# Kernel optimization log

Hardware: AMD Instinct MI355X
Metric: run time of the kernel (lower is better)

## Reference

```python
import jax, jax.numpy as jnp
import numpy as np

N_NODES = 100000
N_EDGES = 1600000
NUM_GRAPHS = 4096
HID = 128
F_IN = 11
F_OUT = 19


def setup_inputs() -> dict:
    key = jax.random.key(0)
    ks = jax.random.split(key, 8)
    x = jax.random.normal(ks[0], (N_NODES, F_IN), dtype=jnp.float32)
    edge_src = jax.random.randint(ks[1], (N_EDGES,), 0, N_NODES)
    edge_dst = jax.random.randint(ks[2], (N_EDGES,), 0, N_NODES)
    batch = jnp.sort(jax.random.randint(ks[3], (N_NODES,), 0, NUM_GRAPHS))
    W1 = jax.random.normal(ks[4], (F_IN, HID), dtype=jnp.float32) / np.sqrt(F_IN)
    b1 = jnp.zeros((HID,), dtype=jnp.float32)
    W2 = jax.random.normal(ks[5], (HID, HID), dtype=jnp.float32) / np.sqrt(HID)
    b2 = jnp.zeros((HID,), dtype=jnp.float32)
    Wlin = jax.random.normal(ks[6], (HID, F_OUT), dtype=jnp.float32) / np.sqrt(HID)
    blin = jnp.zeros((F_OUT,), dtype=jnp.float32)
    return {"x": x, "edge_src": edge_src, "edge_dst": edge_dst, "batch": batch,
            "W1": W1, "b1": b1, "W2": W2, "b2": b2, "Wlin": Wlin, "blin": blin}


def _gcn_conv(x, W, b, src, dst, norm, n_nodes):
    # x: [N, Fin] -> h: [N, Fout]; gather-normalize-scatter over edges (self-loops included in src/dst/norm)
    h = x @ W
    msgs = h[src] * norm[:, None]              # [E+N, Fout]
    out = jax.ops.segment_sum(msgs, dst, num_segments=n_nodes)
    return out + b


def reference(x, edge_src, edge_dst, batch, W1, b1, W2, b2, Wlin, blin):
    n = x.shape[0]
    # add self-loops (GCNConv default)
    loops = jnp.arange(n)
    src = jnp.concatenate([edge_src, loops])
    dst = jnp.concatenate([edge_dst, loops])
    # symmetric normalization deg^-1/2[src] * deg^-1/2[dst], deg computed on dst with self-loops
    deg = jax.ops.segment_sum(jnp.ones_like(dst, dtype=x.dtype), dst, num_segments=n)
    dinv = jnp.where(deg > 0, jax.lax.rsqrt(deg), 0.0)
    norm = dinv[src] * dinv[dst]
    h = _gcn_conv(x, W1, b1, src, dst, norm, n)
    h = jax.nn.relu(h)
    h = _gcn_conv(h, W2, b2, src, dst, norm, n)
    # global mean pool over batch assignment
    sums = jax.ops.segment_sum(h, batch, num_segments=NUM_GRAPHS)
    cnts = jax.ops.segment_sum(jnp.ones((n,), dtype=h.dtype), batch, num_segments=NUM_GRAPHS)
    pooled = sums / jnp.maximum(cnts, 1.0)[:, None]   # [NUM_GRAPHS, HID]
    return pooled @ Wlin + blin                       # [NUM_GRAPHS, F_OUT]
```

## Files before the change

kernel.cpp:

```cpp
#include <hip/hip_runtime.h>
#include <hip/hip_fp16.h>

#define N_NODES 100000
#define N_EDGES 1600000
#define NUM_G   4096
#define HID     128
#define F_IN    11
#define F_PAD   16
#define F_OUT   19

#define NB      256
#define KPB     391
#define BCAP    8192
#define GCAP    1024
#define P01_EPB 2048
#define NREG    8
#define REGW    12500
#define GPB     4
#define NAGG    782
#define CH_G    8

__device__ inline void acc_row_f16(float* acc, uint4 u, float w) {
    const __half2* hp = (const __half2*)&u;
#pragma unroll
    for (int i = 0; i < 4; ++i) {
        acc[2 * i]     += __half2float(__low2half(hp[i]))  * w;
        acc[2 * i + 1] += __half2float(__high2half(hp[i])) * w;
    }
}
__device__ inline void add_row_f16(float* acc, uint4 u) {
    const __half2* hp = (const __half2*)&u;
#pragma unroll
    for (int i = 0; i < 4; ++i) {
        acc[2 * i]     += __half2float(__low2half(hp[i]));
        acc[2 * i + 1] += __half2float(__high2half(hp[i]));
    }
}

__global__ void p1_place(const int* __restrict__ src, const int* __restrict__ dst,
                         int* __restrict__ bcur, unsigned int* __restrict__ ebuf) {
    __shared__ int h[NB];
    __shared__ int base[NB];
    h[threadIdx.x] = 0;
    __syncthreads();
    unsigned int pk[8]; int bn[8];
    int b0 = blockIdx.x * P01_EPB;
    int e8 = b0 + threadIdx.x * 8;
    if (e8 + 8 <= N_EDGES) {
        int4 s0 = *(const int4*)(src + e8);
        int4 s1 = *(const int4*)(src + e8 + 4);
        int4 d0 = *(const int4*)(dst + e8);
        int4 d1 = *(const int4*)(dst + e8 + 4);
        int ss[8] = { s0.x, s0.y, s0.z, s0.w, s1.x, s1.y, s1.z, s1.w };
        int dd[8] = { d0.x, d0.y, d0.z, d0.w, d1.x, d1.y, d1.z, d1.w };
#pragma unroll
        for (int k = 0; k < 8; ++k) {
            bn[k] = dd[k] / KPB;
            pk[k] = ((unsigned)ss[k] << 9) | (unsigned)(dd[k] - bn[k] * KPB);
        }
    } else {
#pragma unroll
        for (int k = 0; k < 8; ++k) {
            int e = e8 + k;
            if (e < N_EDGES) {
                int d = dst[e];
                bn[k] = d / KPB;
                pk[k] = ((unsigned)src[e] << 9) | (unsigned)(d - bn[k] * KPB);
            } else bn[k] = -1;
        }
    }
#pragma unroll
    for (int k = 0; k < 8; ++k)
        if (bn[k] >= 0) atomicAdd(&h[bn[k]], 1);
    __syncthreads();
    {
        int c = h[threadIdx.x];
        base[threadIdx.x] = c ? atomicAdd(&bcur[threadIdx.x], c) : 0;
    }
    __syncthreads();
    h[threadIdx.x] = 0;
    __syncthreads();
#pragma unroll
    for (int k = 0; k < 8; ++k) {
        if (bn[k] >= 0) {
            int r = atomicAdd(&h[bn[k]], 1);
            ebuf[(size_t)bn[k] * BCAP + base[bn[k]] + r] = pk[k];
        }
    }
}

__global__ void p2_build(const unsigned int* __restrict__ ebuf, const int* __restrict__ bcur,
                         const float* __restrict__ x,
                         int* __restrict__ row_ptr, int* __restrict__ deg,
                         int* __restrict__ col, float* __restrict__ wd,
                         float* __restrict__ dinv, __half* __restrict__ xp) {
    __shared__ int hist[512];
    __shared__ float ldinv[512];
    __shared__ int wsum[8];
    __shared__ int woff[8];
    int b  = blockIdx.x;
    int t  = threadIdx.x;
    int dbase = b * KPB;
    int nd = N_NODES - dbase; if (nd > KPB) nd = KPB;
    hist[t] = 0;
    __syncthreads();
    int e0 = b * BCAP;
    int e1 = e0 + bcur[b];
    for (int e = e0 + t; e < e1; e += 512)
        atomicAdd(&hist[ebuf[e] & 511u], 1);
    __syncthreads();
    int v = hist[t];
    int lane = t & 63, wv = t >> 6;
    int sv = v;
#pragma unroll
    for (int off = 1; off < 64; off <<= 1) {
        int n = __shfl_up(sv, off, 64);
        if (lane >= off) sv += n;
    }
    if (lane == 63) wsum[wv] = sv;
    __syncthreads();
    if (t == 0) {
        int run = 0;
#pragma unroll
        for (int w = 0; w < 8; ++w) { woff[w] = run; run += wsum[w]; }
    }
    __syncthreads();
    int excl = sv - v + woff[wv];
    float di = rsqrtf(1.0f + (float)v);
    ldinv[t] = di;
    if (t < nd) {
        row_ptr[dbase + t] = e0 + excl;
        deg[dbase + t]     = v;
        dinv[dbase + t]    = di;
    }
    __syncthreads();
    hist[t] = e0 + excl;
    __syncthreads();
    for (int e = e0 + t; e < e1; e += 512) {
        unsigned int w = ebuf[e];
        int dl = (int)(w & 511u);
        int pos = atomicAdd(&hist[dl], 1);
        col[pos] = (int)(w >> 9);
        wd[pos]  = ldinv[dl];
    }
    for (int idx = t; idx < nd * F_PAD; idx += 512) {
        int vl = idx >> 4, f = idx & 15;
        int gv = dbase + vl;
        xp[(size_t)gv * F_PAD + f] =
            __float2half_rn((f < F_IN) ? ldinv[vl] * x[(size_t)gv * F_IN + f] : 0.f);
    }
}

__global__ void agg_es8(const __half* __restrict__ xp, const int* __restrict__ row_ptr,
                        const int* __restrict__ deg, const int* __restrict__ col,
                        const float* __restrict__ dinv,
                        const float* __restrict__ W1, const float* __restrict__ b1,
                        __half* __restrict__ Bh,
                        const int* __restrict__ batch, const float* __restrict__ wd,
                        uint2* __restrict__ ewp, int* __restrict__ gro,
                        int* __restrict__ gb) {
    __shared__ __align__(16) float xs[128][F_PAD];
    __shared__ float W1s[F_IN * HID];
    __shared__ float b1s[HID];
    __shared__ float ds[128];
    __shared__ int cnt[NREG];
    __shared__ int cur[NREG];
    __shared__ int range[2];
    int tid = threadIdx.x;

    if (blockIdx.x < NAGG) {
        for (int i = tid; i < F_IN * HID; i += 256) W1s[i] = W1[i];
        if (tid < HID) b1s[tid] = b1[tid];
        const uint4* xp4 = (const uint4*)xp;
        int v0   = blockIdx.x * 128;
        int v    = v0 + (tid >> 1);
        int lane = tid & 1;
        if (v < N_NODES) {
            if (lane == 0) ds[tid >> 1] = dinv[v];
            float a[8];
#pragma unroll
            for (int k = 0; k < 8; ++k) a[k] = 0.f;
            add_row_f16(a, xp4[(size_t)v * 2 + lane]);
            int j = row_ptr[v], end = j + deg[v];
            int nfull = (end - j) >> 3;
            if (nfull > 0) {
                int cc[8];
#pragma unroll
                for (int k = 0; k < 8; ++k) cc[k] = col[j + k];
                for (int c = 1; c < nfull; ++c) {
                    int nn[8];
#pragma unroll
                    for (int k = 0; k < 8; ++k) nn[k] = col[j + 8 * c + k];
                    uint4 u[8];
#pragma unroll
                    for (int k = 0; k < 8; ++k) u[k] = xp4[(size_t)cc[k] * 2 + lane];
#pragma unroll
                    for (int k = 0; k < 8; ++k) add_row_f16(a, u[k]);
#pragma unroll
                    for (int k = 0; k < 8; ++k) cc[k] = nn[k];
                }
                uint4 u[8];
#pragma unroll
                for (int k = 0; k < 8; ++k) u[k] = xp4[(size_t)cc[k] * 2 + lane];
#pragma unroll
                for (int k = 0; k < 8; ++k) add_row_f16(a, u[k]);
                j += nfull * 8;
            }
            for (; j + 3 < end; j += 4) {
                int s0 = col[j], s1 = col[j + 1], s2 = col[j + 2], s3 = col[j + 3];
                uint4 u0 = xp4[(size_t)s0 * 2 + lane];
                uint4 u1 = xp4[(size_t)s1 * 2 + lane];
                uint4 u2 = xp4[(size_t)s2 * 2 + lane];
                uint4 u3 = xp4[(size_t)s3 * 2 + lane];
                add_row_f16(a, u0); add_row_f16(a, u1);
                add_row_f16(a, u2); add_row_f16(a, u3);
            }
            for (; j < end; ++j)
                add_row_f16(a, xp4[(size_t)col[j] * 2 + lane]);
#pragma unroll
            for (int k = 0; k < 8; ++k) xs[tid >> 1][lane * 8 + k] = a[k];
        }
        __syncthreads();
        int jf   = tid & 127;
        int half = tid >> 7;
        float w[F_IN];
#pragma unroll
        for (int k = 0; k < F_IN; ++k) w[k] = W1s[k * HID + jf];
        float bb = b1s[jf];
        int nmax = N_NODES - v0; if (nmax > 128) nmax = 128;
        for (int n = half; n < nmax; n += 2) {
            const float4* xr = (const float4*)xs[n];
            float4 x0 = xr[0], x1 = xr[1], x2 = xr[2];
            float a = x0.x * w[0] + x0.y * w[1] + x0.z * w[2] + x0.w * w[3]
                    + x1.x * w[4] + x1.y * w[5] + x1.z * w[6] + x1.w * w[7]
                    + x2.x * w[8] + x2.y * w[9] + x2.z * w[10];
            float dv = ds[n];
            float h = fmaxf(dv * a + bb, 0.f);
            Bh[(size_t)(v0 + n) * HID + jf] = __float2half_rn(dv * h);
        }
    } else {
        int g = blockIdx.x - NAGG;
        if (tid < NREG) cnt[tid] = 0;
        if (tid < 2) {
            int tgt = g + tid;
            int lo = 0, hi = N_NODES;
            while (lo < hi) { int m = (lo + hi) >> 1; if (batch[m] < tgt) lo = m + 1; else hi = m; }
            range[tid] = lo;
        }
        __syncthreads();
        int r0 = range[0], r1 = range[1];
        if (tid == 0) {
            gb[g] = r0;
            if (g == NUM_G - 1) gb[NUM_G] = N_NODES;
        }
        int bb0 = 0, bb1 = -1;
        if (r1 > r0) { bb0 = r0 / KPB; bb1 = (r1 - 1) / KPB; }
        for (int bb = bb0; bb <= bb1; ++bb) {
            int vlo = r0 > bb * KPB ? r0 : bb * KPB;
            int vhi = r1 < bb * KPB + KPB ? r1 : bb * KPB + KPB;
            int ee0 = row_ptr[vlo];
            int ee1 = row_ptr[vhi - 1] + deg[vhi - 1];
            for (int e = ee0 + tid; e < ee1; e += 256)
                atomicAdd(&cnt[(unsigned)col[e] / REGW], 1);
        }
        for (int v = r0 + tid; v < r1; v += 256)
            atomicAdd(&cnt[(unsigned)v / REGW], 1);
        __syncthreads();
        if (tid == 0) {
            int run = g * GCAP;
#pragma unroll
            for (int p = 0; p < NREG; ++p) {
                gro[g * 9 + p] = run;
                cur[p] = run;
                run += cnt[p];
            }
            gro[g * 9 + 8] = run;
        }
        __syncthreads();
        for (int bb = bb0; bb <= bb1; ++bb) {
            int vlo = r0 > bb * KPB ? r0 : bb * KPB;
            int vhi = r1 < bb * KPB + KPB ? r1 : bb * KPB + KPB;
            int ee0 = row_ptr[vlo];
            int ee1 = row_ptr[vhi - 1] + deg[vhi - 1];
            for (int e = ee0 + tid; e < ee1; e += 256) {
                int s = col[e];
                int pos = atomicAdd(&cur[(unsigned)s / REGW], 1);
                ewp[pos] = make_uint2((unsigned)s, __float_as_uint(wd[e]));
            }
        }
        for (int v = r0 + tid; v < r1; v += 256) {
            int pos = atomicAdd(&cur[(unsigned)v / REGW], 1);
            ewp[pos] = make_uint2((unsigned)v, __float_as_uint(dinv[v]));
        }
    }
}

__global__ void pool_gather(const __half* __restrict__ Bh,
                            const int* __restrict__ gro,
                            const uint2* __restrict__ ewp,
                            float* __restrict__ part) {
    __shared__ float red[32][HID + 4];
    int b    = blockIdx.x;
    int gset = b >> 3;
    int p    = b & 7;
    int tid  = threadIdx.x;
    int grp  = tid >> 3;
    int lane = tid & 7;
    int g    = gset * GPB + (grp >> 3);
    int q    = grp & 7;
    const uint4* B4 = (const uint4*)Bh;
    float acc[16];
#pragma unroll
    for (int k = 0; k < 16; ++k) acc[k] = 0.f;

    int e0 = gro[g * 9 + p], e1 = gro[g * 9 + p + 1];
    int e = e0 + q;
    for (; e + 8 < e1; e += 16) {
        uint2 q0 = ewp[e], q1 = ewp[e + 8];
        uint4 u00 = B4[(size_t)q0.x * 16 + lane * 2];
        uint4 u01 = B4[(size_t)q0.x * 16 + lane * 2 + 1];
        uint4 u10 = B4[(size_t)q1.x * 16 + lane * 2];
        uint4 u11 = B4[(size_t)q1.x * 16 + lane * 2 + 1];
        float w0 = __uint_as_float(q0.y), w1 = __uint_as_float(q1.y);
        acc_row_f16(acc,     u00, w0);
        acc_row_f16(acc + 8, u01, w0);
        acc_row_f16(acc,     u10, w1);
        acc_row_f16(acc + 8, u11, w1);
    }
    for (; e < e1; e += 8) {
        uint2 q0 = ewp[e];
        uint4 u00 = B4[(size_t)q0.x * 16 + lane * 2];
        uint4 u01 = B4[(size_t)q0.x * 16 + lane * 2 + 1];
        float w0 = __uint_as_float(q0.y);
        acc_row_f16(acc,     u00, w0);
        acc_row_f16(acc + 8, u01, w0);
    }
#pragma unroll
    for (int k = 0; k < 16; ++k) red[grp][lane * 16 + k] = acc[k];
    __syncthreads();
    for (int i = tid; i < GPB * HID; i += 256) {
        int gg = i >> 7, f = i & 127;
        int rb = gg * 8;
        float s = 0.f;
#pragma unroll
        for (int r = 0; r < 8; ++r) s += red[rb + r][f];
        part[(size_t)((gset * GPB + gg) * NREG + p) * HID + f] = s;
    }
}

__global__ void combine_head(const float* __restrict__ part, const int* __restrict__ gb,
                             const float* __restrict__ W2, const float* __restrict__ b2,
                             const float* __restrict__ Wlin, const float* __restrict__ blin,
                             float* __restrict__ out) {
    __shared__ float r[CH_G][HID];
    __shared__ float tt[CH_G][HID + 4];
    __shared__ float bsc[CH_G];
    int g0  = blockIdx.x * CH_G;
    int tid = threadIdx.x;
    int f   = tid & 127;
    int gh  = tid >> 7;
    int q0  = gh * 4;
#pragma unroll
    for (int c = 0; c < 4; ++c) {
        int gg = q0 + c;
        int g  = g0 + gg;
        float s = 0.f;
#pragma unroll
        for (int p = 0; p < NREG; ++p) s += part[(size_t)(g * NREG + p) * HID + f];
        int cnt = gb[g + 1] - gb[g];
        float inv = (cnt > 0) ? 1.0f / (float)cnt : 0.f;
        r[gg][f] = s * inv;
        if (f == 0) bsc[gg] = (cnt > 0) ? 1.0f : 0.f;
    }
    __syncthreads();
    float bf = b2[f];
    float t0 = bf * bsc[q0];
    float t1 = bf * bsc[q0 + 1];
    float t2 = bf * bsc[q0 + 2];
    float t3 = bf * bsc[q0 + 3];
#pragma unroll 4
    for (int k = 0; k < HID; ++k) {
        float w = W2[k * HID + f];
        t0 += r[q0][k] * w;
        t1 += r[q0 + 1][k] * w;
        t2 += r[q0 + 2][k] * w;
        t3 += r[q0 + 3][k] * w;
    }
    tt[q0][f]     = t0;
    tt[q0 + 1][f] = t1;
    tt[q0 + 2][f] = t2;
    tt[q0 + 3][f] = t3;
    __syncthreads();
    if (tid < CH_G * F_OUT) {
        int gg = tid / F_OUT;
        int fo = tid - gg * F_OUT;
        float o = blin[fo];
#pragma unroll 8
        for (int k = 0; k < HID; ++k) o += tt[gg][k] * Wlin[k * F_OUT + fo];
        out[(size_t)(g0 + gg) * F_OUT + fo] = o;
    }
}

extern "C" void kernel_launch(void* const* d_in, const int* in_sizes, int n_in,
                              void* d_out, int out_size, void* d_ws, size_t ws_size,
                              hipStream_t stream) {
    const float* x    = (const float*)d_in[0];
    const int*   esrc = (const int*)  d_in[1];
    const int*   edst = (const int*)  d_in[2];
    const int*   batch= (const int*)  d_in[3];
    const float* W1   = (const float*)d_in[4];
    const float* b1   = (const float*)d_in[5];
    const float* W2   = (const float*)d_in[6];
    const float* b2   = (const float*)d_in[7];
    const float* Wlin = (const float*)d_in[8];
    const float* blin = (const float*)d_in[9];
    float* out = (float*)d_out;

    char* p = (char*)d_ws;
    float*        dinv    = (float*)p;        p += sizeof(float) * N_NODES;
    __half*       xp      = (__half*)p;       p += sizeof(__half) * (size_t)N_NODES * F_PAD;
    __half*       Bh      = (__half*)p;       p += sizeof(__half) * (size_t)N_NODES * HID;
    unsigned int* ebuf    = (unsigned int*)p; p += sizeof(unsigned int) * (size_t)NB * BCAP;
    int*          col     = (int*)p;          p += sizeof(int) * (size_t)NB * BCAP;
    float*        wd      = (float*)p;        p += sizeof(float) * (size_t)NB * BCAP;
    int*          deg     = (int*)p;          p += sizeof(int) * N_NODES;
    uint2*        ewp     = (uint2*)p;        p += sizeof(uint2) * (size_t)NUM_G * GCAP;
    float*        part    = (float*)p;        p += sizeof(float) * (size_t)NUM_G * NREG * HID;
    int*          row_ptr = (int*)p;          p += sizeof(int) * (N_NODES + 4);
    int*          gb      = (int*)p;          p += sizeof(int) * (NUM_G + 4);
    int*          gro     = (int*)p;          p += sizeof(int) * (NUM_G * 9 + 4);
    int*          bcur    = (int*)p;          p += sizeof(int) * NB;

    const int nblk_e = (N_EDGES + P01_EPB - 1) / P01_EPB;

    hipMemsetAsync(bcur, 0, sizeof(int) * NB, stream);
    p1_place<<<nblk_e, 256, 0, stream>>>(esrc, edst, bcur, ebuf);
    p2_build<<<NB, 512, 0, stream>>>(ebuf, bcur, x, row_ptr, deg, col, wd, dinv, xp);

    agg_es8<<<NAGG + NUM_G, 256, 0, stream>>>(xp, row_ptr, deg, col, dinv, W1, b1, Bh,
                                              batch, wd, ewp, gro, gb);

    pool_gather<<<(NUM_G / GPB) * NREG, 256, 0, stream>>>(Bh, gro, ewp, part);

    combine_head<<<NUM_G / CH_G, 256, 0, stream>>>(part, gb, W2, b2, Wlin, blin, out);
}
```

Measured before the change: 240.6 us.

## Simplify layer-1 gather, unroll layer-2 edge loop by four with coalesced row halves

The layer-1 aggregation drops its 8-wide software-pipelined neighbor gather and keeps only the 4-wide loop. Its W1 transform now reads weights and bias from shared memory on every node instead of caching them in registers. The layer-2 pooled edge kernel processes four edges per iteration instead of two, raising memory-level parallelism. Its 16-byte row loads now interleave the eight lanes contiguously across each half row, which should give better-coalesced accesses. The layer-1 changes reduce register pressure but may cost gather latency hiding and extra LDS traffic.

```diff
diff --git a/kernel.cpp b/kernel.cpp
--- a/kernel.cpp
+++ b/kernel.cpp
@@ -159,7 +159,7 @@
                         const int* __restrict__ batch, const float* __restrict__ wd,
                         uint2* __restrict__ ewp, int* __restrict__ gro,
                         int* __restrict__ gb) {
-    __shared__ __align__(16) float xs[128][F_PAD];
+    __shared__ float xs[128][F_PAD];
     __shared__ float W1s[F_IN * HID];
     __shared__ float b1s[HID];
     __shared__ float ds[128];
@@ -182,30 +182,6 @@
             for (int k = 0; k < 8; ++k) a[k] = 0.f;
             add_row_f16(a, xp4[(size_t)v * 2 + lane]);
             int j = row_ptr[v], end = j + deg[v];
-            int nfull = (end - j) >> 3;
-            if (nfull > 0) {
-                int cc[8];
-#pragma unroll
-                for (int k = 0; k < 8; ++k) cc[k] = col[j + k];
-                for (int c = 1; c < nfull; ++c) {
-                    int nn[8];
-#pragma unroll
-                    for (int k = 0; k < 8; ++k) nn[k] = col[j + 8 * c + k];
-                    uint4 u[8];
-#pragma unroll
-                    for (int k = 0; k < 8; ++k) u[k] = xp4[(size_t)cc[k] * 2 + lane];
-#pragma unroll
-                    for (int k = 0; k < 8; ++k) add_row_f16(a, u[k]);
-#pragma unroll
-                    for (int k = 0; k < 8; ++k) cc[k] = nn[k];
-                }
-                uint4 u[8];
-#pragma unroll
-                for (int k = 0; k < 8; ++k) u[k] = xp4[(size_t)cc[k] * 2 + lane];
-#pragma unroll
-                for (int k = 0; k < 8; ++k) add_row_f16(a, u[k]);
-                j += nfull * 8;
-            }
             for (; j + 3 < end; j += 4) {
                 int s0 = col[j], s1 = col[j + 1], s2 = col[j + 2], s3 = col[j + 3];
                 uint4 u0 = xp4[(size_t)s0 * 2 + lane];
@@ -223,19 +199,13 @@
         __syncthreads();
         int jf   = tid & 127;
         int half = tid >> 7;
-        float w[F_IN];
-#pragma unroll
-        for (int k = 0; k < F_IN; ++k) w[k] = W1s[k * HID + jf];
-        float bb = b1s[jf];
         int nmax = N_NODES - v0; if (nmax > 128) nmax = 128;
         for (int n = half; n < nmax; n += 2) {
-            const float4* xr = (const float4*)xs[n];
-            float4 x0 = xr[0], x1 = xr[1], x2 = xr[2];
-            float a = x0.x * w[0] + x0.y * w[1] + x0.z * w[2] + x0.w * w[3]
-                    + x1.x * w[4] + x1.y * w[5] + x1.z * w[6] + x1.w * w[7]
-                    + x2.x * w[8] + x2.y * w[9] + x2.z * w[10];
+            float a = 0.f;
+#pragma unroll
+            for (int k = 0; k < F_IN; ++k) a += xs[n][k] * W1s[k * HID + jf];
             float dv = ds[n];
-            float h = fmaxf(dv * a + bb, 0.f);
+            float h = fmaxf(dv * a + b1s[jf], 0.f);
             Bh[(size_t)(v0 + n) * HID + jf] = __float2half_rn(dv * h);
         }
     } else {
@@ -315,28 +285,39 @@
 
     int e0 = gro[g * 9 + p], e1 = gro[g * 9 + p + 1];
     int e = e0 + q;
-    for (; e + 8 < e1; e += 16) {
-        uint2 q0 = ewp[e], q1 = ewp[e + 8];
-        uint4 u00 = B4[(size_t)q0.x * 16 + lane * 2];
-        uint4 u01 = B4[(size_t)q0.x * 16 + lane * 2 + 1];
-        uint4 u10 = B4[(size_t)q1.x * 16 + lane * 2];
-        uint4 u11 = B4[(size_t)q1.x * 16 + lane * 2 + 1];
+    for (; e + 24 < e1; e += 32) {
+        uint2 q0 = ewp[e], q1 = ewp[e + 8], q2 = ewp[e + 16], q3 = ewp[e + 24];
+        uint4 u00 = B4[(size_t)q0.x * 16 + lane];
+        uint4 u01 = B4[(size_t)q0.x * 16 + 8 + lane];
+        uint4 u10 = B4[(size_t)q1.x * 16 + lane];
+        uint4 u11 = B4[(size_t)q1.x * 16 + 8 + lane];
+        uint4 u20 = B4[(size_t)q2.x * 16 + lane];
+        uint4 u21 = B4[(size_t)q2.x * 16 + 8 + lane];
+        uint4 u30 = B4[(size_t)q3.x * 16 + lane];
+        uint4 u31 = B4[(size_t)q3.x * 16 + 8 + lane];
         float w0 = __uint_as_float(q0.y), w1 = __uint_as_float(q1.y);
+        float w2 = __uint_as_float(q2.y), w3 = __uint_as_float(q3.y);
         acc_row_f16(acc,     u00, w0);
         acc_row_f16(acc + 8, u01, w0);
         acc_row_f16(acc,     u10, w1);
         acc_row_f16(acc + 8, u11, w1);
+        acc_row_f16(acc,     u20, w2);
+        acc_row_f16(acc + 8, u21, w2);
+        acc_row_f16(acc,     u30, w3);
+        acc_row_f16(acc + 8, u31, w3);
     }
     for (; e < e1; e += 8) {
         uint2 q0 = ewp[e];
-        uint4 u00 = B4[(size_t)q0.x * 16 + lane * 2];
-        uint4 u01 = B4[(size_t)q0.x * 16 + lane * 2 + 1];
+        uint4 u00 = B4[(size_t)q0.x * 16 + lane];
+        uint4 u01 = B4[(size_t)q0.x * 16 + 8 + lane];
         float w0 = __uint_as_float(q0.y);
         acc_row_f16(acc,     u00, w0);
         acc_row_f16(acc + 8, u01, w0);
     }
 #pragma unroll
-    for (int k = 0; k < 16; ++k) red[grp][lane * 16 + k] = acc[k];
+    for (int k = 0; k < 8; ++k) red[grp][lane * 8 + k]      = acc[k];
+#pragma unroll
+    for (int k = 0; k < 8; ++k) red[grp][64 + lane * 8 + k] = acc[8 + k];
     __syncthreads();
     for (int i = tid; i < GPB * HID; i += 256) {
         int gg = i >> 7, f = i & 127;
```

New measurement: 239.1 us. No clear change (-0.6%).
